# Performance work log

Hardware: AMD Instinct MI355X
Metric: run time of the kernel (lower is better)

## Reference

```python
import jax, jax.numpy as jnp
import numpy as np

D_MODEL, D_STATE, D_CONV = 768, 8, 3
D_INNER = D_MODEL  # expand = 1
BATCH, SEQ = 4, 8192


def setup_inputs() -> dict:
    key = jax.random.key(0)
    ks = jax.random.split(key, 7)
    x = jax.random.normal(ks[0], (BATCH, SEQ, D_MODEL), dtype=jnp.float32)
    W_in = jax.random.normal(ks[1], (D_MODEL, 2 * D_INNER), dtype=jnp.float32) * 0.02
    conv_w = jax.random.normal(ks[2], (D_INNER, 1, D_CONV), dtype=jnp.float32) * 0.1
    conv_b = jnp.zeros((D_INNER,), dtype=jnp.float32)
    B = jax.random.normal(ks[3], (D_INNER, D_STATE), dtype=jnp.float32)
    C = jax.random.normal(ks[4], (D_INNER, D_STATE), dtype=jnp.float32)
    D = jnp.ones((D_INNER,), dtype=jnp.float32)
    W_out = jax.random.normal(ks[5], (D_INNER, D_MODEL), dtype=jnp.float32) * 0.02
    return {"x": x, "W_in": W_in, "conv_w": conv_w, "conv_b": conv_b,
            "B": B, "C": C, "D": D, "W_out": W_out}


def _forward(x, W_in, conv_w, conv_b, B, C, D, W_out):
    # in_proj and chunk
    xz = x @ W_in                                   # [B, L, 2*d_inner]
    xc, z = jnp.split(xz, 2, axis=-1)               # each [B, L, d_inner]
    # depthwise causal conv1d: torch pads (d_conv-1) both sides then slices [:L]
    # == left-pad (d_conv-1), no right pad
    xc = jnp.transpose(xc, (0, 2, 1))               # [B, d_inner, L]
    xc = jax.lax.conv_general_dilated(
        xc, conv_w,
        window_strides=(1,), padding=[(D_CONV - 1, 0)],
        dimension_numbers=("NCH", "OIH", "NCH"),
        feature_group_count=D_INNER)
    xc = xc + conv_b[None, :, None]
    xc = jnp.transpose(xc, (0, 2, 1))               # [B, L, d_inner]
    xc = jax.nn.silu(xc)
    z = jax.nn.silu(z)
    # simple SSM: h_t = h_{t-1} + outer(u_t, B); y_t = sum_s h_t*C + u_t*D
    # => y = cumsum_t(u) * sum_s(B*C) + u*D   (exact algebraic identity)
    BC = jnp.sum(B * C, axis=-1)                    # [d_inner]
    y = jnp.cumsum(xc, axis=1) * BC + xc * D
    out = (y * z) @ W_out                           # [B, L, d_model]
    return out


def reference(x, W_in, conv_w, conv_b, B, C, D, W_out):
    return _forward(x, W_in, conv_w, conv_b, B, C, D, W_out)
```

## Files before the change

### kernel.cpp

```cpp
#include <hip/hip_runtime.h>
#include <hip/hip_bf16.h>

#define D_MODEL 768
#define NSEQ    8192
#define NBATCH  4
#define MROWS   (NBATCH*NSEQ)
#define CHUNK   128
#define NCHUNK  (NSEQ/CHUNK)

#define BM 128
#define BN 192
#define BK 64

typedef __attribute__((ext_vector_type(8)))  short bshort8;
typedef __attribute__((ext_vector_type(16))) float f32x16;

__device__ __forceinline__ float bf2f(ushort u){
  union { unsigned int i; float f; } x; x.i = ((unsigned int)u) << 16; return x.f;
}
__device__ __forceinline__ ushort f2bf(float f){
  union { float f; unsigned int i; } x; x.f = f;
  unsigned int r = x.i + 0x7fffu + ((x.i >> 16) & 1u);
  return (ushort)(r >> 16);
}
__device__ __forceinline__ float silu_f(float v){ return v / (1.0f + __expf(-v)); }

__device__ __forceinline__ void async_copy16(const ushort* g, ushort* l){
  __builtin_amdgcn_global_load_lds((const __attribute__((address_space(1))) void*)g,
                                   (__attribute__((address_space(3))) void*)l, 16, 0, 0);
}

__global__ void tr_cvt(const float* __restrict__ in, ushort* __restrict__ out, int R, int C){
  __shared__ float tile[32][33];
  int c0 = blockIdx.x*32, r0 = blockIdx.y*32;
  int tx = threadIdx.x & 31, ty = threadIdx.x >> 5;
  #pragma unroll
  for (int p=0;p<4;p++){
    int r = ty + p*8;
    tile[r][tx] = in[(size_t)(r0+r)*C + c0 + tx];
  }
  __syncthreads();
  #pragma unroll
  for (int p=0;p<4;p++){
    int c = ty + p*8;
    out[(size_t)(c0+c)*R + r0 + tx] = f2bf(tile[tx][c]);
  }
}

__global__ void cvt_bf16(const float* __restrict__ in, ushort* __restrict__ out, int n){
  int i = (blockIdx.x*256 + threadIdx.x)*8;
  if (i >= n) return;
  const float4 f0 = *(const float4*)(in + i);
  const float4 f1 = *(const float4*)(in + i + 4);
  ushort o[8];
  o[0]=f2bf(f0.x); o[1]=f2bf(f0.y); o[2]=f2bf(f0.z); o[3]=f2bf(f0.w);
  o[4]=f2bf(f1.x); o[5]=f2bf(f1.y); o[6]=f2bf(f1.z); o[7]=f2bf(f1.w);
  *(ulonglong2*)(out + i) = *(const ulonglong2*)o;
}

template<int MODE>
__global__ __launch_bounds__(256) void gemm_bt(
    const ushort* __restrict__ A, const ushort* __restrict__ BT,
    ushort* __restrict__ oxc, ushort* __restrict__ oz, float* __restrict__ of,
    int K)
{
  __shared__ __align__(16) ushort Asm[BM*BK];
  __shared__ __align__(16) ushort Bsm[BN*BK];
  const int tid = threadIdx.x;
  const int bm = blockIdx.x, bn = blockIdx.y;
  const int lane = tid & 63, wid = tid >> 6;
  const int wm = (wid >> 1) * 64, wn = (wid & 1) * 96;
  const int l31 = lane & 31, half = lane >> 5;

  const ushort* Ag[4]; ushort* Al[4];
  #pragma unroll
  for (int it=0; it<4; ++it){
    int p  = it*256 + tid;
    int r  = p >> 3;
    int cl = (p & 7) ^ (r & 7);
    Ag[it] = A + (size_t)(bm*BM + r)*K + cl*8;
    Al[it] = Asm + p*8;
  }
  const ushort* Bg[6]; ushort* Bl[6];
  #pragma unroll
  for (int it=0; it<6; ++it){
    int p  = it*256 + tid;
    int r  = p >> 3;
    int cl = (p & 7) ^ (r & 7);
    Bg[it] = BT + (size_t)(bn*BN + r)*K + cl*8;
    Bl[it] = Bsm + p*8;
  }

  int arow[2], ar7[2], brow[3], br7[3];
  #pragma unroll
  for (int i=0;i<2;i++){
    int ra = wm + i*32 + l31; arow[i] = ra*BK; ar7[i] = ra & 7;
  }
  #pragma unroll
  for (int j=0;j<3;j++){
    int rb = wn + j*32 + l31; brow[j] = rb*BK; br7[j] = rb & 7;
  }

  f32x16 acc[2][3];
  #pragma unroll
  for (int i=0;i<2;i++)
    #pragma unroll
    for (int j=0;j<3;j++)
      #pragma unroll
      for (int r=0;r<16;r++) acc[i][j][r] = 0.f;

  const int KT = K / BK;
  for (int kt=0; kt<KT; ++kt){
    __syncthreads();
    #pragma unroll
    for (int it=0; it<4; ++it){ async_copy16(Ag[it], Al[it]); Ag[it] += BK; }
    #pragma unroll
    for (int it=0; it<6; ++it){ async_copy16(Bg[it], Bl[it]); Bg[it] += BK; }
    asm volatile("s_waitcnt vmcnt(0)" ::: "memory");
    __syncthreads();

    #pragma unroll
    for (int s=0; s<4; ++s){
      const int cbase = s*2 + half;
      bshort8 av[2], bv[3];
      #pragma unroll
      for (int i=0;i<2;i++)
        av[i] = *(const bshort8*)(Asm + arow[i] + ((cbase ^ ar7[i]) << 3));
      #pragma unroll
      for (int j=0;j<3;j++)
        bv[j] = *(const bshort8*)(Bsm + brow[j] + ((cbase ^ br7[j]) << 3));
      #pragma unroll
      for (int i=0;i<2;i++)
        #pragma unroll
        for (int j=0;j<3;j++)
          acc[i][j] = __builtin_amdgcn_mfma_f32_32x32x16_bf16(av[i], bv[j], acc[i][j], 0,0,0);
    }
  }

  if (MODE==0 && bn < 4){
    #pragma unroll
    for (int i=0;i<2;i++){
      const int Rbase = bm*BM + wm + i*32 + 4*half;
      #pragma unroll
      for (int j=0;j<3;j++){
        const int Cc = bn*BN + wn + j*32 + l31;
        #pragma unroll
        for (int reg=0; reg<16; reg++){
          const int R = Rbase + (reg & 3) + 8*(reg >> 2);
          oxc[(size_t)R*768 + Cc] = f2bf(acc[i][j][reg]);
        }
      }
    }
  } else if (MODE==0){
    #pragma unroll
    for (int i=0;i<2;i++){
      const int Rbase = bm*BM + wm + i*32 + 4*half;
      #pragma unroll
      for (int j=0;j<3;j++){
        const int Cc = bn*BN - 768 + wn + j*32 + l31;
        #pragma unroll
        for (int reg=0; reg<16; reg++){
          const int R = Rbase + (reg & 3) + 8*(reg >> 2);
          oz[(size_t)R*768 + Cc] = f2bf(silu_f(acc[i][j][reg]));
        }
      }
    }
  } else {
    #pragma unroll
    for (int i=0;i<2;i++){
      const int Rbase = bm*BM + wm + i*32 + 4*half;
      #pragma unroll
      for (int j=0;j<3;j++){
        const int Cc = bn*BN + wn + j*32 + l31;
        #pragma unroll
        for (int reg=0; reg<16; reg++){
          const int R = Rbase + (reg & 3) + 8*(reg >> 2);
          of[(size_t)R*768 + Cc] = acc[i][j][reg];
        }
      }
    }
  }
}

__global__ void conv_psum(const ushort* __restrict__ xc, const float* __restrict__ cw,
                          const float* __restrict__ cb, float* __restrict__ psum){
  int c = blockIdx.y*256 + threadIdx.x;
  int b = blockIdx.z, ch = blockIdx.x;
  int t0 = ch*CHUNK;
  const ushort* xp = xc + (size_t)b*NSEQ*768 + c;
  float w0=cw[c*3+0], w1=cw[c*3+1], w2=cw[c*3+2], bb=cb[c];
  float xm2 = (t0>=2) ? bf2f(xp[(size_t)(t0-2)*768]) : 0.f;
  float xm1 = (t0>=1) ? bf2f(xp[(size_t)(t0-1)*768]) : 0.f;
  float s = 0.f;
  #pragma unroll 4
  for (int i=0;i<CHUNK;i++){
    float x0 = bf2f(xp[(size_t)(t0+i)*768]);
    float pre = w0*xm2 + w1*xm1 + w2*x0 + bb;
    s += silu_f(pre);
    xm2 = xm1; xm1 = x0;
  }
  psum[((size_t)b*NCHUNK + ch)*768 + c] = s;
}

__global__ void scan_chunks(const float* __restrict__ psum, float* __restrict__ offs){
  int idx = blockIdx.x*256 + threadIdx.x;
  int b = idx/768, c = idx%768;
  float run = 0.f;
  for (int ch=0; ch<NCHUNK; ch++){
    size_t o = ((size_t)b*NCHUNK + ch)*768 + c;
    offs[o] = run;
    run += psum[o];
  }
}

__global__ void scan_apply(const ushort* __restrict__ xc, const ushort* __restrict__ zb,
                           const float* __restrict__ cw, const float* __restrict__ cb,
                           const float* __restrict__ Bm, const float* __restrict__ Cm,
                           const float* __restrict__ Dv, const float* __restrict__ offs,
                           ushort* __restrict__ v){
  int c = blockIdx.y*256 + threadIdx.x;
  int b = blockIdx.z, ch = blockIdx.x;
  int t0 = ch*CHUNK;
  size_t base = (size_t)b*NSEQ*768 + c;
  const ushort* xp = xc + base;
  const ushort* zp = zb + base;
  ushort* vp = v + base;
  float w0=cw[c*3+0], w1=cw[c*3+1], w2=cw[c*3+2], bb=cb[c];
  float bc = 0.f;
  #pragma unroll
  for (int s=0;s<8;s++) bc += Bm[c*8+s]*Cm[c*8+s];
  float dd = Dv[c];
  float cum = offs[((size_t)b*NCHUNK + ch)*768 + c];
  float xm2 = (t0>=2) ? bf2f(xp[(size_t)(t0-2)*768]) : 0.f;
  float xm1 = (t0>=1) ? bf2f(xp[(size_t)(t0-1)*768]) : 0.f;
  #pragma unroll 4
  for (int i=0;i<CHUNK;i++){
    size_t o = (size_t)(t0+i)*768;
    float x0 = bf2f(xp[o]);
    float pre = w0*xm2 + w1*xm1 + w2*x0 + bb;
    float u = silu_f(pre);
    cum += u;
    float y = bc*cum + dd*u;
    vp[o] = f2bf(y * bf2f(zp[o]));
    xm2 = xm1; xm1 = x0;
  }
}

extern "C" void kernel_launch(void* const* d_in, const int* in_sizes, int n_in,
                              void* d_out, int out_size, void* d_ws, size_t ws_size,
                              hipStream_t stream)
{
  const float* x      = (const float*)d_in[0];
  const float* W_in   = (const float*)d_in[1];
  const float* conv_w = (const float*)d_in[2];
  const float* conv_b = (const float*)d_in[3];
  const float* Bm     = (const float*)d_in[4];
  const float* Cm     = (const float*)d_in[5];
  const float* Dv     = (const float*)d_in[6];
  const float* W_out  = (const float*)d_in[7];
  float* out = (float*)d_out;

  char* ws = (char*)d_ws;
  ushort* xbf   = (ushort*)(ws + 0);
  ushort* xcbf  = (ushort*)(ws + 50331648);
  ushort* zbf   = (ushort*)(ws + 100663296);
  ushort* wint  = (ushort*)(ws + 150994944);
  ushort* woutt = (ushort*)(ws + 153354240);
  float*  psum  = (float*)(ws + 154533888);
  float*  offs  = (float*)(ws + 155320320);
  if (ws_size < 156106752) return;

  tr_cvt<<<dim3(1536/32, 768/32), 256, 0, stream>>>(W_in,  wint,  768, 1536);
  tr_cvt<<<dim3(768/32,  768/32), 256, 0, stream>>>(W_out, woutt, 768, 768);
  cvt_bf16<<<(MROWS*768)/2048, 256, 0, stream>>>(x, xbf, MROWS*768);

  gemm_bt<0><<<dim3(MROWS/BM, 1536/BN), 256, 0, stream>>>(xbf, wint, xcbf, zbf, nullptr, 768);

  conv_psum  <<<dim3(NCHUNK, 3, NBATCH), 256, 0, stream>>>(xcbf, conv_w, conv_b, psum);
  scan_chunks<<<12, 256, 0, stream>>>(psum, offs);
  scan_apply <<<dim3(NCHUNK, 3, NBATCH), 256, 0, stream>>>(xcbf, zbf, conv_w, conv_b,
                                                           Bm, Cm, Dv, offs, xbf );

  gemm_bt<1><<<dim3(MROWS/BM, 768/BN), 256, 0, stream>>>(xbf, woutt, nullptr, nullptr, out, 768);
}
```

Baseline: 414.1 us.

## Double-buffer GEMM LDS tiles with async prefetch and shrink tiles to 128x128x32

Restructures the bf16 MFMA GEMM so the next K-tile's global-to-LDS async copies are issued before computing on the current buffer, waiting only on the older loads. Tile sizes shrink to BN=128 and BK=32 with a new XOR swizzle, and launch bounds request 4 blocks per SM for higher occupancy. The aim is to hide global load latency behind MFMA work. Smaller tiles lower per-block reuse and raise barrier count per unit of work. The host launch grid must also match the new BN, which is not visible here.

```diff
diff --git a/kernel.cpp b/kernel.cpp
--- a/kernel.cpp
+++ b/kernel.cpp
@@ -9,8 +9,8 @@
 #define NCHUNK  (NSEQ/CHUNK)
 
 #define BM 128
-#define BN 192
-#define BK 64
+#define BN 128
+#define BK 32
 
 typedef __attribute__((ext_vector_type(8)))  short bshort8;
 typedef __attribute__((ext_vector_type(16))) float f32x16;
@@ -59,90 +59,89 @@
 }
 
 template<int MODE>
-__global__ __launch_bounds__(256) void gemm_bt(
+__global__ __launch_bounds__(256, 4) void gemm_bt(
     const ushort* __restrict__ A, const ushort* __restrict__ BT,
     ushort* __restrict__ oxc, ushort* __restrict__ oz, float* __restrict__ of,
     int K)
 {
-  __shared__ __align__(16) ushort Asm[BM*BK];
-  __shared__ __align__(16) ushort Bsm[BN*BK];
+  __shared__ __align__(16) ushort Asm[2*BM*BK];
+  __shared__ __align__(16) ushort Bsm[2*BM*BK];
   const int tid = threadIdx.x;
   const int bm = blockIdx.x, bn = blockIdx.y;
   const int lane = tid & 63, wid = tid >> 6;
-  const int wm = (wid >> 1) * 64, wn = (wid & 1) * 96;
+  const int wm = (wid >> 1) * 64, wn = (wid & 1) * 64;
   const int l31 = lane & 31, half = lane >> 5;
 
-  const ushort* Ag[4]; ushort* Al[4];
-  #pragma unroll
-  for (int it=0; it<4; ++it){
+  const ushort* AgB[2]; const ushort* BgB[2]; int AlO[2], BlO[2];
+  #pragma unroll
+  for (int it=0; it<2; ++it){
     int p  = it*256 + tid;
-    int r  = p >> 3;
-    int cl = (p & 7) ^ (r & 7);
-    Ag[it] = A + (size_t)(bm*BM + r)*K + cl*8;
-    Al[it] = Asm + p*8;
-  }
-  const ushort* Bg[6]; ushort* Bl[6];
-  #pragma unroll
-  for (int it=0; it<6; ++it){
-    int p  = it*256 + tid;
-    int r  = p >> 3;
-    int cl = (p & 7) ^ (r & 7);
-    Bg[it] = BT + (size_t)(bn*BN + r)*K + cl*8;
-    Bl[it] = Bsm + p*8;
-  }
-
-  int arow[2], ar7[2], brow[3], br7[3];
+    int r  = p >> 2;
+    int cl = (p & 3) ^ ((r >> 1) & 3);
+    AgB[it] = A  + (size_t)(bm*BM + r)*K + cl*8;
+    BgB[it] = BT + (size_t)(bn*BN + r)*K + cl*8;
+    AlO[it] = p*8;
+    BlO[it] = p*8;
+  }
+
+  int arow[2], asz[2], brow[2], bsz[2];
   #pragma unroll
   for (int i=0;i<2;i++){
-    int ra = wm + i*32 + l31; arow[i] = ra*BK; ar7[i] = ra & 7;
-  }
-  #pragma unroll
-  for (int j=0;j<3;j++){
-    int rb = wn + j*32 + l31; brow[j] = rb*BK; br7[j] = rb & 7;
-  }
-
-  f32x16 acc[2][3];
+    int ra = wm + i*32 + l31; arow[i] = ra*BK; asz[i] = (ra >> 1) & 3;
+    int rb = wn + i*32 + l31; brow[i] = rb*BK; bsz[i] = (rb >> 1) & 3;
+  }
+
+  f32x16 acc[2][2];
   #pragma unroll
   for (int i=0;i<2;i++)
     #pragma unroll
-    for (int j=0;j<3;j++)
+    for (int j=0;j<2;j++)
       #pragma unroll
       for (int r=0;r<16;r++) acc[i][j][r] = 0.f;
 
   const int KT = K / BK;
+
+  #pragma unroll
+  for (int it=0; it<2; ++it){ async_copy16(AgB[it], Asm + AlO[it]); }
+  #pragma unroll
+  for (int it=0; it<2; ++it){ async_copy16(BgB[it], Bsm + BlO[it]); }
+
   for (int kt=0; kt<KT; ++kt){
-    __syncthreads();
-    #pragma unroll
-    for (int it=0; it<4; ++it){ async_copy16(Ag[it], Al[it]); Ag[it] += BK; }
-    #pragma unroll
-    for (int it=0; it<6; ++it){ async_copy16(Bg[it], Bl[it]); Bg[it] += BK; }
-    asm volatile("s_waitcnt vmcnt(0)" ::: "memory");
-    __syncthreads();
-
-    #pragma unroll
-    for (int s=0; s<4; ++s){
-      const int cbase = s*2 + half;
-      bshort8 av[2], bv[3];
-      #pragma unroll
-      for (int i=0;i<2;i++)
-        av[i] = *(const bshort8*)(Asm + arow[i] + ((cbase ^ ar7[i]) << 3));
-      #pragma unroll
-      for (int j=0;j<3;j++)
-        bv[j] = *(const bshort8*)(Bsm + brow[j] + ((cbase ^ br7[j]) << 3));
-      #pragma unroll
-      for (int i=0;i<2;i++)
-        #pragma unroll
-        for (int j=0;j<3;j++)
-          acc[i][j] = __builtin_amdgcn_mfma_f32_32x32x16_bf16(av[i], bv[j], acc[i][j], 0,0,0);
-    }
-  }
-
-  if (MODE==0 && bn < 4){
+    const int cur = kt & 1;
+    const int nxt = cur ^ 1;
+    asm volatile("s_barrier" ::: "memory");
+    const int kn = (kt+1 < KT) ? (kt+1)*BK : 0;
+    #pragma unroll
+    for (int it=0; it<2; ++it){ async_copy16(AgB[it] + kn, Asm + nxt*BM*BK + AlO[it]); }
+    #pragma unroll
+    for (int it=0; it<2; ++it){ async_copy16(BgB[it] + kn, Bsm + nxt*BM*BK + BlO[it]); }
+    asm volatile("s_waitcnt vmcnt(4)" ::: "memory");
+    asm volatile("s_barrier" ::: "memory");
+
+    const ushort* Ab = Asm + cur*BM*BK;
+    const ushort* Bb = Bsm + cur*BM*BK;
+    #pragma unroll
+    for (int s=0; s<2; ++s){
+      const int c = s*2 + half;
+      bshort8 av[2], bv[2];
+      #pragma unroll
+      for (int i=0;i<2;i++){
+        av[i] = *(const bshort8*)(Ab + arow[i] + ((c ^ asz[i]) << 3));
+        bv[i] = *(const bshort8*)(Bb + brow[i] + ((c ^ bsz[i]) << 3));
+      }
+      acc[0][0] = __builtin_amdgcn_mfma_f32_32x32x16_bf16(av[0], bv[0], acc[0][0], 0,0,0);
+      acc[0][1] = __builtin_amdgcn_mfma_f32_32x32x16_bf16(av[0], bv[1], acc[0][1], 0,0,0);
+      acc[1][0] = __builtin_amdgcn_mfma_f32_32x32x16_bf16(av[1], bv[0], acc[1][0], 0,0,0);
+      acc[1][1] = __builtin_amdgcn_mfma_f32_32x32x16_bf16(av[1], bv[1], acc[1][1], 0,0,0);
+    }
+  }
+
+  if (MODE==0 && bn < 6){
     #pragma unroll
     for (int i=0;i<2;i++){
       const int Rbase = bm*BM + wm + i*32 + 4*half;
       #pragma unroll
-      for (int j=0;j<3;j++){
+      for (int j=0;j<2;j++){
         const int Cc = bn*BN + wn + j*32 + l31;
         #pragma unroll
         for (int reg=0; reg<16; reg++){
@@ -156,7 +155,7 @@
     for (int i=0;i<2;i++){
       const int Rbase = bm*BM + wm + i*32 + 4*half;
       #pragma unroll
-      for (int j=0;j<3;j++){
+      for (int j=0;j<2;j++){
         const int Cc = bn*BN - 768 + wn + j*32 + l31;
         #pragma unroll
         for (int reg=0; reg<16; reg++){
@@ -170,7 +169,7 @@
     for (int i=0;i<2;i++){
       const int Rbase = bm*BM + wm + i*32 + 4*half;
       #pragma unroll
-      for (int j=0;j<3;j++){
+      for (int j=0;j<2;j++){
         const int Cc = bn*BN + wn + j*32 + l31;
         #pragma unroll
         for (int reg=0; reg<16; reg++){
```

Result: slower. 427.5 us (+3.2%).
